# Kernel tuning notes

Measured on AMD Instinct MI355X. Metric: run time of the kernel, lower is better.

The kernel has to match this reference:

```python
import jax, jax.numpy as jnp
import numpy as np

EMBED_DIM = 1024
NUM_HEADS = 16
HEAD_DIM = EMBED_DIM // NUM_HEADS
LAMBDA_ENTANGLE = 0.35


def setup_inputs() -> dict:
    key = jax.random.key(0)
    ks = jax.random.split(key, 10)
    B, S, D = 2, 2048, EMBED_DIM
    init = 1.0 / np.sqrt(D)  # mimic nn.Linear uniform init scale
    x = jax.random.normal(ks[0], (B, S, D), dtype=jnp.float32)
    Wq = jax.random.uniform(ks[1], (D, D), jnp.float32, -init, init)
    bq = jax.random.uniform(ks[2], (D,), jnp.float32, -init, init)
    Wk = jax.random.uniform(ks[3], (D, D), jnp.float32, -init, init)
    bk = jax.random.uniform(ks[4], (D,), jnp.float32, -init, init)
    Wv = jax.random.uniform(ks[5], (D, D), jnp.float32, -init, init)
    bv = jax.random.uniform(ks[6], (D,), jnp.float32, -init, init)
    Wo = jax.random.uniform(ks[7], (D, D), jnp.float32, -init, init)
    bo = jax.random.uniform(ks[8], (D,), jnp.float32, -init, init)
    J_attn = jax.random.normal(ks[9], (NUM_HEADS, HEAD_DIM, HEAD_DIM), dtype=jnp.float32) * 0.02
    lambda_attn = jnp.asarray(LAMBDA_ENTANGLE, dtype=jnp.float32)
    return {"x": x, "Wq": Wq, "bq": bq, "Wk": Wk, "bk": bk, "Wv": Wv, "bv": bv,
            "Wo": Wo, "bo": bo, "J_attn": J_attn, "lambda_attn": lambda_attn}


def reference(x, Wq, bq, Wk, bk, Wv, bv, Wo, bo, J_attn, lambda_attn):
    B, S, D = x.shape
    H, Hd = NUM_HEADS, HEAD_DIM
    scale = jnp.sqrt(jnp.asarray(Hd, dtype=x.dtype))

    def heads(W, b):
        # (B,S,D) @ (D,D) + b -> (B,H,S,Hd)
        y = jnp.einsum('bsd,ed->bse', x, W) + b
        return y.reshape(B, S, H, Hd).transpose(0, 2, 1, 3)

    Q = heads(Wq, bq)
    K = heads(Wk, bk)
    V = heads(Wv, bv)

    scores = jnp.einsum('bhid,bhjd->bhij', Q, K) / scale
    # bilinear entanglement correction: tanh(Q) J tanh(K)^T
    QJ = jnp.einsum('bhid,hde->bhie', jnp.tanh(Q), J_attn)  # (B,H,S,Hd)
    delta = jnp.einsum('bhie,bhje->bhij', QJ, jnp.tanh(K))
    scores = scores + lambda_attn * delta

    causal = jnp.triu(jnp.ones((S, S), dtype=bool), k=1)
    scores = jnp.where(causal, -jnp.inf, scores)

    probs = jax.nn.softmax(scores, axis=-1)
    out = jnp.einsum('bhij,bhjd->bhid', probs, V)  # (B,H,S,Hd)
    out = out.transpose(0, 2, 1, 3).reshape(B, S, D)
    return jnp.einsum('bsd,ed->bse', out, Wo) + bo
```

## Files before the change

### kernel.cpp

```cpp
#include <hip/hip_runtime.h>
#include <hip/hip_bf16.h>

typedef unsigned short u16;
typedef __bf16 bf16x8 __attribute__((ext_vector_type(8)));
typedef float f32x4 __attribute__((ext_vector_type(4)));
typedef unsigned short u16x4 __attribute__((ext_vector_type(4)));

#define MFMA16(a, b, c) __builtin_amdgcn_mfma_f32_16x16x32_bf16(a, b, c, 0, 0, 0)

#define EMB 1024
#define SEQ 2048
#define NH 16
#define HD 64
#define LOG2E 1.4426950408889634f

#define GLOAD_LDS16(g, l) __builtin_amdgcn_global_load_lds( \
    (const __attribute__((address_space(1))) unsigned int*)(g), \
    (__attribute__((address_space(3))) unsigned int*)(l), 16, 0, 0)

__device__ __forceinline__ float b2f(u16 u) {
    union { unsigned int i; float f; } v; v.i = ((unsigned int)u) << 16; return v.f;
}
__device__ __forceinline__ u16 f2b(float f) {
    __hip_bfloat16 h = __float2bfloat16(f);
    return *reinterpret_cast<u16*>(&h);
}
__device__ __forceinline__ u16x4 pack4(float a, float b, float c, float d) {
    union { __hip_bfloat162 h2[2]; u16x4 u; } r;
    r.h2[0] = __float22bfloat162_rn(float2{a, b});
    r.h2[1] = __float22bfloat162_rn(float2{c, d});
    return r.u;
}
__device__ __forceinline__ bf16x8 ldfrag(const u16* p) {
    return *reinterpret_cast<const bf16x8*>(p);
}
__device__ __forceinline__ bf16x8 cvt8(const float* p) {
    const float4 a = *reinterpret_cast<const float4*>(p);
    const float4 b = *reinterpret_cast<const float4*>(p + 4);
    union { u16x4 q[2]; bf16x8 v; } r;
    r.q[0] = pack4(a.x, a.y, a.z, a.w);
    r.q[1] = pack4(b.x, b.y, b.z, b.w);
    return r.v;
}
__device__ __forceinline__ float fast_tanh(float x) {
    float t = __builtin_amdgcn_exp2f(x * (2.0f * LOG2E));
    return 1.0f - 2.0f * __builtin_amdgcn_rcpf(t + 1.0f);
}

__global__ __launch_bounds__(256) void cvt_all(
        const float* __restrict__ x,  const float* __restrict__ Wq,
        const float* __restrict__ Wk, const float* __restrict__ Wv,
        const float* __restrict__ Wo, const float* __restrict__ J,
        u16* __restrict__ dst)
{
    size_t i = ((size_t)blockIdx.x * 256 + threadIdx.x) * 8;
    const float* src; size_t off; u16* d;
    if (i < 4194304) { src = x; off = i; d = dst + i; }
    else if (i < 8388608) {
        size_t j = i - 4194304; int w = (int)(j >> 20); off = j & 1048575;
        src = (w == 0) ? Wq : (w == 1) ? Wk : (w == 2) ? Wv : Wo;
        d = dst + i;
    } else {
        off = i - 8388608; src = J; d = dst + 29360128 + off;
    }
    *(bf16x8*)d = cvt8(src + off);
}

__global__ __launch_bounds__(512) void qkv_fused(
        const u16* __restrict__ A,
        const u16* __restrict__ W0, const float* __restrict__ B0,
        const u16* __restrict__ W1, const float* __restrict__ B1,
        const u16* __restrict__ W2, const float* __restrict__ B2,
        const float* __restrict__ lam, const u16* __restrict__ Jb,
        u16* __restrict__ Qa, u16* __restrict__ Ka, u16* __restrict__ Vt)
{
    __shared__ __attribute__((aligned(16))) u16 sS[2][4][128 * 64];

    const int t = threadIdx.x;
    const int w = t >> 6, L = t & 63;
    const int wm = w >> 1, wn = w & 1;
    const int lr = L & 15, lq = L >> 4;
    const int m0 = blockIdx.y * 128, n0 = blockIdx.x * 128;

    const int c0r = t >> 3,  c0o = ((t & 7) ^ (c0r & 7)) * 8;
    const int c1  = 512 + t;
    const int c1r = c1 >> 3, c1o = ((c1 & 7) ^ (c1r & 7)) * 8;
    const u16* s0p[4], * s1p[4];
    s0p[0] = A  + (size_t)(m0 + c0r) * EMB + c0o;
    s0p[1] = W0 + (size_t)(n0 + c0r) * EMB + c0o;
    s0p[2] = W1 + (size_t)(n0 + c0r) * EMB + c0o;
    s0p[3] = W2 + (size_t)(n0 + c0r) * EMB + c0o;
    s1p[0] = A  + (size_t)(m0 + c1r) * EMB + c1o;
    s1p[1] = W0 + (size_t)(n0 + c1r) * EMB + c1o;
    s1p[2] = W1 + (size_t)(n0 + c1r) * EMB + c1o;
    s1p[3] = W2 + (size_t)(n0 + c1r) * EMB + c1o;

    f32x4 acc[3][2][4];
#pragma unroll
    for (int z = 0; z < 3; z++)
#pragma unroll
        for (int i = 0; i < 2; i++)
#pragma unroll
            for (int j = 0; j < 4; j++) { f32x4 zr = {0.f,0.f,0.f,0.f}; acc[z][i][j] = zr; }

    {
        int4 r0[4], r1[4];
#pragma unroll
        for (int mat = 0; mat < 4; mat++) { r0[mat] = *(const int4*)s0p[mat];
                                            r1[mat] = *(const int4*)s1p[mat]; }
#pragma unroll
        for (int mat = 0; mat < 4; mat++) {
            *(int4*)&sS[0][mat][(size_t)t * 8]  = r0[mat];
            *(int4*)&sS[0][mat][(size_t)c1 * 8] = r1[mat];
        }
    }
    __syncthreads();

    int cur = 0;
    for (int k0 = 0; k0 < EMB; k0 += 64) {
        const bool pf = (k0 + 64) < EMB;
        int4 r0[4], r1[4];
        if (pf) {
#pragma unroll
            for (int mat = 0; mat < 4; mat++) {
                r0[mat] = *(const int4*)(s0p[mat] + k0 + 64);
                r1[mat] = *(const int4*)(s1p[mat] + k0 + 64);
            }
        }
        __builtin_amdgcn_s_setprio(1);
#pragma unroll
        for (int s = 0; s < 2; s++) {
            bf16x8 af[2];
#pragma unroll
            for (int mi = 0; mi < 2; mi++) {
                int row = wm * 32 + mi * 16 + lr;
                af[mi] = ldfrag(&sS[cur][0][(row * 8 + ((s * 4 + lq) ^ (row & 7))) * 8]);
            }
#pragma unroll
            for (int z = 0; z < 3; z++) {
                bf16x8 bfr[4];
#pragma unroll
                for (int ni = 0; ni < 4; ni++) {
                    int row = wn * 64 + ni * 16 + lr;
                    bfr[ni] = ldfrag(
                        &sS[cur][1 + z][(row * 8 + ((s * 4 + lq) ^ (row & 7))) * 8]);
                }
#pragma unroll
                for (int mi = 0; mi < 2; mi++)
#pragma unroll
                    for (int ni = 0; ni < 4; ni++)
                        acc[z][mi][ni] = MFMA16(bfr[ni], af[mi], acc[z][mi][ni]);
            }
        }
        __builtin_amdgcn_s_setprio(0);
        if (pf) {
#pragma unroll
            for (int mat = 0; mat < 4; mat++) {
                *(int4*)&sS[cur ^ 1][mat][(size_t)t * 8]  = r0[mat];
                *(int4*)&sS[cur ^ 1][mat][(size_t)c1 * 8] = r1[mat];
            }
        }
        __syncthreads();
        cur ^= 1;
    }

    u16* sU = &sS[0][0][(size_t)w * 2048];

    const float lamf = lam[0];
    const float qsc = 0.125f * LOG2E, lsc = lamf * LOG2E;
    const float* biases[3] = {B0, B1, B2};
#pragma unroll
    for (int z = 0; z < 3; z++)
#pragma unroll
        for (int mi = 0; mi < 2; mi++)
#pragma unroll
            for (int ni = 0; ni < 4; ni++) {
                const int sg = m0 + wm * 32 + mi * 16 + lr;
                const int ng = n0 + wn * 64 + ni * 16 + lq * 4;
                const float4 bv4 = *(const float4*)&biases[z][ng];
                const float v0 = acc[z][mi][ni][0] + bv4.x;
                const float v1 = acc[z][mi][ni][1] + bv4.y;
                const float v2 = acc[z][mi][ni][2] + bv4.z;
                const float v3 = acc[z][mi][ni][3] + bv4.w;
                const int b = sg >> 11, s0 = sg & 2047;
                const int h = ng >> 6, d0 = ng & 63;
                if (z == 0) {
                    size_t i128 = ((size_t)(b * NH + h) * SEQ + s0) * 128 + d0;
                    *(u16x4*)&Qa[i128] = pack4(v0 * qsc, v1 * qsc, v2 * qsc, v3 * qsc);
                    *(u16x4*)&Qa[i128 + 64] =
                        pack4(lsc * fast_tanh(v0), lsc * fast_tanh(v1),
                              lsc * fast_tanh(v2), lsc * fast_tanh(v3));
                } else if (z == 1) {
                    *(u16x4*)&Ka[((size_t)(b * NH + h) * SEQ + s0) * 128 + d0] =
                        pack4(v0, v1, v2, v3);
                    const int sl = mi * 16 + lr;
                    const int chunk = (d0 >> 3) ^ (sl & 7);
                    *(u16x4*)&sU[sl * 64 + chunk * 8 + (d0 & 7)] =
                        pack4(fast_tanh(v0), fast_tanh(v1),
                              fast_tanh(v2), fast_tanh(v3));
                } else {
#pragma unroll
                    for (int r = 0; r < 4; r++) {
                        float vr = (r == 0) ? v0 : (r == 1) ? v1 : (r == 2) ? v2 : v3;
                        Vt[((size_t)(b * NH + h) * HD + d0 + r) * SEQ + s0] = f2b(vr);
                    }
                }
            }

    {
        const int hn = (n0 >> 6) + wn;
        const u16* Jh = Jb + (size_t)hn * 4096;
        bf16x8 jf[4][2];
#pragma unroll
        for (int nt = 0; nt < 4; nt++)
#pragma unroll
            for (int s2 = 0; s2 < 2; s2++)
                jf[nt][s2] = ldfrag(&Jh[(nt * 16 + lr) * 64 + s2 * 32 + lq * 8]);
#pragma unroll
        for (int rt2 = 0; rt2 < 2; rt2++) {
            const int r32 = rt2 * 16 + lr;
            bf16x8 a0 = ldfrag(&sU[r32 * 64 + ((0 + lq) ^ (r32 & 7)) * 8]);
            bf16x8 a1 = ldfrag(&sU[r32 * 64 + ((4 + lq) ^ (r32 & 7)) * 8]);
            const int grow = m0 + wm * 32 + rt2 * 16 + lr;
            const int bb = grow >> 11, ss = grow & 2047;
            const size_t kbase = ((size_t)(bb * NH + hn) * SEQ + ss) * 128 + 64;
#pragma unroll
            for (int nt = 0; nt < 4; nt++) {
                f32x4 acc2 = {0.f, 0.f, 0.f, 0.f};
                acc2 = MFMA16(jf[nt][0], a0, acc2);
                acc2 = MFMA16(jf[nt][1], a1, acc2);
                *(u16x4*)&Ka[kbase + nt * 16 + lq * 4] =
                    pack4(acc2[0], acc2[1], acc2[2], acc2[3]);
            }
        }
    }
}

template<int MI>
__global__ __launch_bounds__(256, 4) void gemm_epi(
        const u16* __restrict__ A,
        const u16* __restrict__ W0, const float* __restrict__ B0,
        float* __restrict__ out)
{
    const u16* W = W0; const float* bias = B0;

    __shared__ __attribute__((aligned(16))) u16 sA[MI * 32 * 64];
    __shared__ __attribute__((aligned(16))) u16 sB[128 * 64];

    const int t = threadIdx.x;
    const int w = t >> 6, L = t & 63;
    const int wm = w >> 1, wn = w & 1;
    const int lr = L & 15, lq = L >> 4;
    const int wbase = t & 192;
    const int m0 = blockIdx.y * (MI * 32), n0 = blockIdx.x * 128;

    f32x4 acc[MI][4];
#pragma unroll
    for (int i = 0; i < MI; i++)
#pragma unroll
        for (int j = 0; j < 4; j++) { f32x4 z = {0.f, 0.f, 0.f, 0.f}; acc[i][j] = z; }

    for (int k0 = 0; k0 < EMB; k0 += 64) {
        __syncthreads();
#pragma unroll
        for (int q = 0; q < MI; q++) {
            int c = q * 256 + t;
            int row = c >> 3, cc = c & 7;
            int col8 = cc ^ (row & 7);
            GLOAD_LDS16(&A[(size_t)(m0 + row) * EMB + k0 + col8 * 8],
                        &sA[(q * 256 + wbase) * 8]);
        }
#pragma unroll
        for (int q = 0; q < 4; q++) {
            int c = q * 256 + t;
            int row = c >> 3, cc = c & 7;
            int col8 = cc ^ (row & 7);
            GLOAD_LDS16(&W[(size_t)(n0 + row) * EMB + k0 + col8 * 8],
                        &sB[(q * 256 + wbase) * 8]);
        }
        __syncthreads();
#pragma unroll
        for (int s = 0; s < 2; s++) {
            bf16x8 af[MI], bfr[4];
#pragma unroll
            for (int mi = 0; mi < MI; mi++) {
                int row = wm * (MI * 16) + mi * 16 + lr;
                af[mi] = ldfrag(&sA[(row * 8 + ((s * 4 + lq) ^ (row & 7))) * 8]);
            }
#pragma unroll
            for (int ni = 0; ni < 4; ni++) {
                int row = wn * 64 + ni * 16 + lr;
                bfr[ni] = ldfrag(&sB[(row * 8 + ((s * 4 + lq) ^ (row & 7))) * 8]);
            }
#pragma unroll
            for (int mi = 0; mi < MI; mi++)
#pragma unroll
                for (int ni = 0; ni < 4; ni++)
                    acc[mi][ni] = MFMA16(bfr[ni], af[mi], acc[mi][ni]);
        }
    }

#pragma unroll
    for (int mi = 0; mi < MI; mi++)
#pragma unroll
        for (int ni = 0; ni < 4; ni++) {
            const int sg = m0 + wm * (MI * 16) + mi * 16 + lr;
            const int ng = n0 + wn * 64 + ni * 16 + lq * 4;
            const float4 bv4 = *(const float4*)&bias[ng];
            float4 o = {acc[mi][ni][0] + bv4.x, acc[mi][ni][1] + bv4.y,
                        acc[mi][ni][2] + bv4.z, acc[mi][ni][3] + bv4.w};
            *(float4*)&out[(size_t)sg * EMB + ng] = o;
        }
}

__global__ __launch_bounds__(512) void flash(
        const u16* __restrict__ Qa, const u16* __restrict__ Ka,
        const u16* __restrict__ Vt, u16* __restrict__ attn)
{
    __shared__ __attribute__((aligned(16))) u16 sK[2][128 * 128];
    __shared__ __attribute__((aligned(16))) u16 sVt[2][64 * 128];
    __shared__ __attribute__((aligned(16))) u16 sP[128 * 136];
    __shared__ float sLs[2][4][64][2];

    const int t = threadIdx.x, w = t >> 6, L = t & 63, lr = L & 15, lq = L >> 4;
    const int wq = w & 3, wk = w >> 2;
    const int bh = blockIdx.x & 31, p = blockIdx.x >> 5;
    const int i_l = wq * 16 + lr;
    const u16* Kbase = Ka + (size_t)bh * SEQ * 128;
    const u16* Vbase = Vt + (size_t)bh * HD * SEQ;
    const int b = bh >> 4, h = bh & 15;
    float* sOt = reinterpret_cast<float*>(sK);

    const u16* kq[4];
#pragma unroll
    for (int q = 0; q < 4; q++) {
        int c = q * 512 + t;
        int row = c >> 4, cc = c & 15;
        kq[q] = Kbase + (size_t)row * 128 + (cc ^ (row & 15)) * 8;
    }
    const u16* vq[2];
#pragma unroll
    for (int q = 0; q < 2; q++) {
        int c = q * 512 + t;
        int d = c >> 4, cc = c & 15;
        vq[q] = Vbase + (size_t)d * SEQ + (cc ^ (d & 7)) * 8;
    }

#pragma unroll 1
    for (int seg = 0; seg < 2; seg++) {
        const int qt = seg ? 15 - p : p;
        const int qm = qt * 128;

        bf16x8 qf[2][4];
#pragma unroll
        for (int g = 0; g < 2; g++) {
            const u16* qrow = Qa + ((size_t)bh * SEQ + qm + g * 64 + i_l) * 128;
#pragma unroll
            for (int s = 0; s < 4; s++) qf[g][s] = ldfrag(qrow + s * 32 + lq * 8);
        }

        f32x4 Ot[2][4];
#pragma unroll
        for (int g = 0; g < 2; g++)
#pragma unroll
            for (int i = 0; i < 4; i++) { f32x4 z = {0.f, 0.f, 0.f, 0.f}; Ot[g][i] = z; }
        float lsum[2] = {0.f, 0.f};

        {
            int4 a0 = *(const int4*)kq[0];
            int4 a1 = *(const int4*)kq[1];
            int4 a2 = *(const int4*)kq[2];
            int4 a3 = *(const int4*)kq[3];
            int4 b0 = *(const int4*)vq[0];
            int4 b1 = *(const int4*)vq[1];
            *(int4*)&sK[0][(size_t)(0 * 512 + t) * 8] = a0;
            *(int4*)&sK[0][(size_t)(1 * 512 + t) * 8] = a1;
            *(int4*)&sK[0][(size_t)(2 * 512 + t) * 8] = a2;
            *(int4*)&sK[0][(size_t)(3 * 512 + t) * 8] = a3;
            *(int4*)&sVt[0][(size_t)(0 * 512 + t) * 8] = b0;
            *(int4*)&sVt[0][(size_t)(1 * 512 + t) * 8] = b1;
        }
        __syncthreads();

        int cur = 0;
        for (int kt = 0; kt <= qt; kt++) {
            const bool pf = kt < qt;
            int4 rk0, rk1, rk2, rk3, rv0, rv1;
            if (pf) {
                const int kn = (kt + 1) * 128;
                rk0 = *(const int4*)(kq[0] + (size_t)kn * 128);
                rk1 = *(const int4*)(kq[1] + (size_t)kn * 128);
                rk2 = *(const int4*)(kq[2] + (size_t)kn * 128);
                rk3 = *(const int4*)(kq[3] + (size_t)kn * 128);
                rv0 = *(const int4*)(vq[0] + kn);
                rv1 = *(const int4*)(vq[1] + kn);
            }
            const u16* sKc = sK[cur];
            const u16* sVc = sVt[cur];

            f32x4 sc[2][4];
#pragma unroll
            for (int g = 0; g < 2; g++)
#pragma unroll
                for (int m = 0; m < 4; m++) { f32x4 z = {0.f,0.f,0.f,0.f}; sc[g][m] = z; }
            __builtin_amdgcn_s_setprio(1);
#pragma unroll
            for (int mt2 = 0; mt2 < 4; mt2++) {
                int j = wk * 64 + mt2 * 16 + lr;
#pragma unroll
                for (int s = 0; s < 4; s++) {
                    bf16x8 kf = ldfrag(&sKc[(j * 16 + ((s * 4 + lq) ^ (j & 15))) * 8]);
                    sc[0][mt2] = MFMA16(kf, qf[0][s], sc[0][mt2]);
                    sc[1][mt2] = MFMA16(kf, qf[1][s], sc[1][mt2]);
                }
            }
            __builtin_amdgcn_s_setprio(0);
            if (kt == qt) {
#pragma unroll
                for (int mt2 = 0; mt2 < 4; mt2++)
#pragma unroll
                    for (int r = 0; r < 4; r++) {
                        int jj = wk * 64 + mt2 * 16 + lq * 4 + r;
                        if (jj > i_l)      sc[0][mt2][r] = -INFINITY;
                        if (jj > 64 + i_l) sc[1][mt2][r] = -INFINITY;
                    }
            }
#pragma unroll
            for (int g = 0; g < 2; g++) {
#pragma unroll
                for (int mt2 = 0; mt2 < 4; mt2++) {
                    float e0 = __builtin_amdgcn_exp2f(sc[g][mt2][0]);
                    float e1 = __builtin_amdgcn_exp2f(sc[g][mt2][1]);
                    float e2 = __builtin_amdgcn_exp2f(sc[g][mt2][2]);
                    float e3 = __builtin_amdgcn_exp2f(sc[g][mt2][3]);
                    lsum[g] += (e0 + e1) + (e2 + e3);
                    *(u16x4*)&sP[(g * 64 + i_l) * 136 + wk * 64 + mt2 * 16 + lq * 4] =
                        pack4(e0, e1, e2, e3);
                }
            }
            __builtin_amdgcn_s_setprio(1);
#pragma unroll
            for (int s2l = 0; s2l < 2; s2l++) {
                bf16x8 pf0 = ldfrag(&sP[(i_l) * 136 + wk * 64 + s2l * 32 + lq * 8]);
                bf16x8 pf1 = ldfrag(&sP[(64 + i_l) * 136 + wk * 64 + s2l * 32 + lq * 8]);
#pragma unroll
                for (int mt = 0; mt < 4; mt++) {
                    int d = mt * 16 + lr;
                    bf16x8 vf = ldfrag(
                        &sVc[(d * 16 + ((wk * 8 + s2l * 4 + lq) ^ (d & 7))) * 8]);
                    Ot[0][mt] = MFMA16(vf, pf0, Ot[0][mt]);
                    Ot[1][mt] = MFMA16(vf, pf1, Ot[1][mt]);
                }
            }
            __builtin_amdgcn_s_setprio(0);
            if (pf) {
                *(int4*)&sK[cur ^ 1][(size_t)(0 * 512 + t) * 8] = rk0;
                *(int4*)&sK[cur ^ 1][(size_t)(1 * 512 + t) * 8] = rk1;
                *(int4*)&sK[cur ^ 1][(size_t)(2 * 512 + t) * 8] = rk2;
                *(int4*)&sK[cur ^ 1][(size_t)(3 * 512 + t) * 8] = rk3;
                *(int4*)&sVt[cur ^ 1][(size_t)(0 * 512 + t) * 8] = rv0;
                *(int4*)&sVt[cur ^ 1][(size_t)(1 * 512 + t) * 8] = rv1;
            }
            __syncthreads();
            cur ^= 1;
        }

#pragma unroll
        for (int g = 0; g < 2; g++) {
            lsum[g] += __shfl_xor(lsum[g], 16);
            lsum[g] += __shfl_xor(lsum[g], 32);
            sLs[wk][wq][L][g] = lsum[g];
        }
        if (wk == 1) {
            float* dst = &sOt[wq * 64 + L];
#pragma unroll
            for (int g = 0; g < 2; g++)
#pragma unroll
                for (int mt = 0; mt < 4; mt++)
#pragma unroll
                    for (int r = 0; r < 4; r++)
                        dst[256 * (g * 16 + mt * 4 + r)] = Ot[g][mt][r];
        }
        __syncthreads();
        if (wk == 0) {
            const float* src = &sOt[wq * 64 + L];
#pragma unroll
            for (int g = 0; g < 2; g++) {
                float ls = lsum[g] + sLs[1][wq][L][g];
                const float r0 = __builtin_amdgcn_rcpf(ls);
                const float inv = r0 * (2.0f - ls * r0);
                const size_t base =
                    ((size_t)(b * SEQ + qm + g * 64 + i_l)) * EMB + h * HD;
#pragma unroll
                for (int mt = 0; mt < 4; mt++)
                    *(u16x4*)&attn[base + mt * 16 + lq * 4] = pack4(
                        (Ot[g][mt][0] + src[256 * (g * 16 + mt * 4 + 0)]) * inv,
                        (Ot[g][mt][1] + src[256 * (g * 16 + mt * 4 + 1)]) * inv,
                        (Ot[g][mt][2] + src[256 * (g * 16 + mt * 4 + 2)]) * inv,
                        (Ot[g][mt][3] + src[256 * (g * 16 + mt * 4 + 3)]) * inv);
            }
        }
        __syncthreads();
    }
}

extern "C" void kernel_launch(void* const* d_in, const int* in_sizes, int n_in,
                              void* d_out, int out_size, void* d_ws, size_t ws_size,
                              hipStream_t stream)
{
    const float* x   = (const float*)d_in[0];
    const float* Wq  = (const float*)d_in[1];
    const float* bq  = (const float*)d_in[2];
    const float* Wk  = (const float*)d_in[3];
    const float* bk  = (const float*)d_in[4];
    const float* Wv  = (const float*)d_in[5];
    const float* bv  = (const float*)d_in[6];
    const float* Wo  = (const float*)d_in[7];
    const float* bo  = (const float*)d_in[8];
    const float* J   = (const float*)d_in[9];
    const float* lam = (const float*)d_in[10];

    u16* ws  = (u16*)d_ws;
    u16* xb  = ws;
    u16* Wqb = xb  + (size_t)4096 * 1024;
    u16* Wkb = Wqb + (size_t)1024 * 1024;
    u16* Wvb = Wkb + (size_t)1024 * 1024;
    u16* Wob = Wvb + (size_t)1024 * 1024;
    u16* Qa  = Wob + (size_t)1024 * 1024;
    u16* Ka  = Qa  + (size_t)32 * 2048 * 128;
    u16* Vt  = Ka  + (size_t)32 * 2048 * 128;
    u16* Jb  = Vt  + (size_t)32 * 64 * 2048;
    u16* attn = xb;
    float* dout = (float*)d_out;

    dim3 blk(256);
    cvt_all<<<dim3(4128), blk, 0, stream>>>(x, Wq, Wk, Wv, Wo, J, ws);
    qkv_fused<<<dim3(8, 32), dim3(512), 0, stream>>>(
        xb, Wqb, bq, Wkb, bk, Wvb, bv, lam, Jb, Qa, Ka, Vt);
    flash<<<dim3(256), dim3(512), 0, stream>>>(Qa, Ka, Vt, attn);
    gemm_epi<2><<<dim3(8, 64), blk, 0, stream>>>(attn, Wob, bo, dout);
}
```

Baseline: 221.4 us.

## Split fused QKV GEMM into per-projection blocks with smaller tiles

Replaces the fused QKV kernel, where each 512-thread block computed all three projections for a 128x128 tile, with a 256-thread kernel that takes the projection index from blockIdx.z and covers a 64x128 tile. The grid grows from 256 to 1536 blocks and per-thread accumulator and LDS use shrink, so occupancy and load balance across CUs should improve. The cost is that the activation tile is no longer shared across Q, K and V, so it is reloaded three times. The software pipeline also changes: sched_barriers replace setprio, and the last iteration issues a redundant load instead of a branch.

```diff
diff --git a/kernel.cpp b/kernel.cpp
--- a/kernel.cpp
+++ b/kernel.cpp
@@ -66,7 +66,7 @@
     *(bf16x8*)d = cvt8(src + off);
 }
 
-__global__ __launch_bounds__(512) void qkv_fused(
+__global__ __launch_bounds__(256, 3) void qkv_gemm(
         const u16* __restrict__ A,
         const u16* __restrict__ W0, const float* __restrict__ B0,
         const u16* __restrict__ W1, const float* __restrict__ B1,
@@ -74,140 +74,142 @@
         const float* __restrict__ lam, const u16* __restrict__ Jb,
         u16* __restrict__ Qa, u16* __restrict__ Ka, u16* __restrict__ Vt)
 {
-    __shared__ __attribute__((aligned(16))) u16 sS[2][4][128 * 64];
+    const int mode = blockIdx.z;
+    const u16* W; const float* bias;
+    if (mode == 0)      { W = W0; bias = B0; }
+    else if (mode == 1) { W = W1; bias = B1; }
+    else                { W = W2; bias = B2; }
+
+    __shared__ __attribute__((aligned(16))) u16 sA[2][64 * 64];
+    __shared__ __attribute__((aligned(16))) u16 sB[2][128 * 64];
 
     const int t = threadIdx.x;
     const int w = t >> 6, L = t & 63;
     const int wm = w >> 1, wn = w & 1;
     const int lr = L & 15, lq = L >> 4;
-    const int m0 = blockIdx.y * 128, n0 = blockIdx.x * 128;
-
-    const int c0r = t >> 3,  c0o = ((t & 7) ^ (c0r & 7)) * 8;
-    const int c1  = 512 + t;
-    const int c1r = c1 >> 3, c1o = ((c1 & 7) ^ (c1r & 7)) * 8;
-    const u16* s0p[4], * s1p[4];
-    s0p[0] = A  + (size_t)(m0 + c0r) * EMB + c0o;
-    s0p[1] = W0 + (size_t)(n0 + c0r) * EMB + c0o;
-    s0p[2] = W1 + (size_t)(n0 + c0r) * EMB + c0o;
-    s0p[3] = W2 + (size_t)(n0 + c0r) * EMB + c0o;
-    s1p[0] = A  + (size_t)(m0 + c1r) * EMB + c1o;
-    s1p[1] = W0 + (size_t)(n0 + c1r) * EMB + c1o;
-    s1p[2] = W1 + (size_t)(n0 + c1r) * EMB + c1o;
-    s1p[3] = W2 + (size_t)(n0 + c1r) * EMB + c1o;
-
-    f32x4 acc[3][2][4];
-#pragma unroll
-    for (int z = 0; z < 3; z++)
-#pragma unroll
-        for (int i = 0; i < 2; i++)
-#pragma unroll
-            for (int j = 0; j < 4; j++) { f32x4 zr = {0.f,0.f,0.f,0.f}; acc[z][i][j] = zr; }
+    const int m0 = blockIdx.y * 64, n0 = blockIdx.x * 128;
+
+    const u16* aptr[2];
+#pragma unroll
+    for (int q = 0; q < 2; q++) {
+        int c = q * 256 + t;
+        int row = c >> 3, col8 = (c & 7) ^ (row & 7);
+        aptr[q] = &A[(size_t)(m0 + row) * EMB + col8 * 8];
+    }
+    const u16* bptr[4];
+#pragma unroll
+    for (int q = 0; q < 4; q++) {
+        int c = q * 256 + t;
+        int row = c >> 3, col8 = (c & 7) ^ (row & 7);
+        bptr[q] = &W[(size_t)(n0 + row) * EMB + col8 * 8];
+    }
+
+    f32x4 acc[2][4];
+#pragma unroll
+    for (int i = 0; i < 2; i++)
+#pragma unroll
+        for (int j = 0; j < 4; j++) { f32x4 z = {0.f, 0.f, 0.f, 0.f}; acc[i][j] = z; }
 
     {
-        int4 r0[4], r1[4];
-#pragma unroll
-        for (int mat = 0; mat < 4; mat++) { r0[mat] = *(const int4*)s0p[mat];
-                                            r1[mat] = *(const int4*)s1p[mat]; }
-#pragma unroll
-        for (int mat = 0; mat < 4; mat++) {
-            *(int4*)&sS[0][mat][(size_t)t * 8]  = r0[mat];
-            *(int4*)&sS[0][mat][(size_t)c1 * 8] = r1[mat];
-        }
+        int4 ra0 = *(const int4*)aptr[0];
+        int4 ra1 = *(const int4*)aptr[1];
+        int4 rb0 = *(const int4*)bptr[0];
+        int4 rb1 = *(const int4*)bptr[1];
+        int4 rb2 = *(const int4*)bptr[2];
+        int4 rb3 = *(const int4*)bptr[3];
+        *(int4*)&sA[0][(size_t)(0 * 256 + t) * 8] = ra0;
+        *(int4*)&sA[0][(size_t)(1 * 256 + t) * 8] = ra1;
+        *(int4*)&sB[0][(size_t)(0 * 256 + t) * 8] = rb0;
+        *(int4*)&sB[0][(size_t)(1 * 256 + t) * 8] = rb1;
+        *(int4*)&sB[0][(size_t)(2 * 256 + t) * 8] = rb2;
+        *(int4*)&sB[0][(size_t)(3 * 256 + t) * 8] = rb3;
     }
     __syncthreads();
 
     int cur = 0;
     for (int k0 = 0; k0 < EMB; k0 += 64) {
-        const bool pf = (k0 + 64) < EMB;
-        int4 r0[4], r1[4];
-        if (pf) {
-#pragma unroll
-            for (int mat = 0; mat < 4; mat++) {
-                r0[mat] = *(const int4*)(s0p[mat] + k0 + 64);
-                r1[mat] = *(const int4*)(s1p[mat] + k0 + 64);
-            }
-        }
-        __builtin_amdgcn_s_setprio(1);
+        const int kn = (k0 + 64 < EMB) ? (k0 + 64) : k0;
+        int4 ra0 = *(const int4*)(aptr[0] + kn);
+        int4 ra1 = *(const int4*)(aptr[1] + kn);
+        int4 rb0 = *(const int4*)(bptr[0] + kn);
+        int4 rb1 = *(const int4*)(bptr[1] + kn);
+        int4 rb2 = *(const int4*)(bptr[2] + kn);
+        int4 rb3 = *(const int4*)(bptr[3] + kn);
+        __builtin_amdgcn_sched_barrier(0);
+
+        const u16* sAc = sA[cur];
+        const u16* sBc = sB[cur];
 #pragma unroll
         for (int s = 0; s < 2; s++) {
-            bf16x8 af[2];
+            bf16x8 af[2], bfr[4];
 #pragma unroll
             for (int mi = 0; mi < 2; mi++) {
                 int row = wm * 32 + mi * 16 + lr;
-                af[mi] = ldfrag(&sS[cur][0][(row * 8 + ((s * 4 + lq) ^ (row & 7))) * 8]);
-            }
-#pragma unroll
-            for (int z = 0; z < 3; z++) {
-                bf16x8 bfr[4];
-#pragma unroll
-                for (int ni = 0; ni < 4; ni++) {
-                    int row = wn * 64 + ni * 16 + lr;
-                    bfr[ni] = ldfrag(
-                        &sS[cur][1 + z][(row * 8 + ((s * 4 + lq) ^ (row & 7))) * 8]);
-                }
-#pragma unroll
-                for (int mi = 0; mi < 2; mi++)
-#pragma unroll
-                    for (int ni = 0; ni < 4; ni++)
-                        acc[z][mi][ni] = MFMA16(bfr[ni], af[mi], acc[z][mi][ni]);
-            }
-        }
-        __builtin_amdgcn_s_setprio(0);
-        if (pf) {
-#pragma unroll
-            for (int mat = 0; mat < 4; mat++) {
-                *(int4*)&sS[cur ^ 1][mat][(size_t)t * 8]  = r0[mat];
-                *(int4*)&sS[cur ^ 1][mat][(size_t)c1 * 8] = r1[mat];
-            }
-        }
+                af[mi] = ldfrag(&sAc[(row * 8 + ((s * 4 + lq) ^ (row & 7))) * 8]);
+            }
+#pragma unroll
+            for (int ni = 0; ni < 4; ni++) {
+                int row = wn * 64 + ni * 16 + lr;
+                bfr[ni] = ldfrag(&sBc[(row * 8 + ((s * 4 + lq) ^ (row & 7))) * 8]);
+            }
+#pragma unroll
+            for (int mi = 0; mi < 2; mi++)
+#pragma unroll
+                for (int ni = 0; ni < 4; ni++)
+                    acc[mi][ni] = MFMA16(bfr[ni], af[mi], acc[mi][ni]);
+        }
+        __builtin_amdgcn_sched_barrier(0);
+        *(int4*)&sA[cur ^ 1][(size_t)(0 * 256 + t) * 8] = ra0;
+        *(int4*)&sA[cur ^ 1][(size_t)(1 * 256 + t) * 8] = ra1;
+        *(int4*)&sB[cur ^ 1][(size_t)(0 * 256 + t) * 8] = rb0;
+        *(int4*)&sB[cur ^ 1][(size_t)(1 * 256 + t) * 8] = rb1;
+        *(int4*)&sB[cur ^ 1][(size_t)(2 * 256 + t) * 8] = rb2;
+        *(int4*)&sB[cur ^ 1][(size_t)(3 * 256 + t) * 8] = rb3;
         __syncthreads();
         cur ^= 1;
     }
 
-    u16* sU = &sS[0][0][(size_t)w * 2048];
+    u16* sU = &sB[0][(size_t)w * 2048];
 
     const float lamf = lam[0];
     const float qsc = 0.125f * LOG2E, lsc = lamf * LOG2E;
-    const float* biases[3] = {B0, B1, B2};
-#pragma unroll
-    for (int z = 0; z < 3; z++)
-#pragma unroll
-        for (int mi = 0; mi < 2; mi++)
-#pragma unroll
-            for (int ni = 0; ni < 4; ni++) {
-                const int sg = m0 + wm * 32 + mi * 16 + lr;
-                const int ng = n0 + wn * 64 + ni * 16 + lq * 4;
-                const float4 bv4 = *(const float4*)&biases[z][ng];
-                const float v0 = acc[z][mi][ni][0] + bv4.x;
-                const float v1 = acc[z][mi][ni][1] + bv4.y;
-                const float v2 = acc[z][mi][ni][2] + bv4.z;
-                const float v3 = acc[z][mi][ni][3] + bv4.w;
-                const int b = sg >> 11, s0 = sg & 2047;
-                const int h = ng >> 6, d0 = ng & 63;
-                if (z == 0) {
-                    size_t i128 = ((size_t)(b * NH + h) * SEQ + s0) * 128 + d0;
-                    *(u16x4*)&Qa[i128] = pack4(v0 * qsc, v1 * qsc, v2 * qsc, v3 * qsc);
-                    *(u16x4*)&Qa[i128 + 64] =
-                        pack4(lsc * fast_tanh(v0), lsc * fast_tanh(v1),
-                              lsc * fast_tanh(v2), lsc * fast_tanh(v3));
-                } else if (z == 1) {
-                    *(u16x4*)&Ka[((size_t)(b * NH + h) * SEQ + s0) * 128 + d0] =
-                        pack4(v0, v1, v2, v3);
-                    const int sl = mi * 16 + lr;
-                    const int chunk = (d0 >> 3) ^ (sl & 7);
-                    *(u16x4*)&sU[sl * 64 + chunk * 8 + (d0 & 7)] =
-                        pack4(fast_tanh(v0), fast_tanh(v1),
-                              fast_tanh(v2), fast_tanh(v3));
-                } else {
-#pragma unroll
-                    for (int r = 0; r < 4; r++) {
-                        float vr = (r == 0) ? v0 : (r == 1) ? v1 : (r == 2) ? v2 : v3;
-                        Vt[((size_t)(b * NH + h) * HD + d0 + r) * SEQ + s0] = f2b(vr);
-                    }
+#pragma unroll
+    for (int mi = 0; mi < 2; mi++)
+#pragma unroll
+        for (int ni = 0; ni < 4; ni++) {
+            const int sg = m0 + wm * 32 + mi * 16 + lr;
+            const int ng = n0 + wn * 64 + ni * 16 + lq * 4;
+            const float4 bv4 = *(const float4*)&bias[ng];
+            const float v0 = acc[mi][ni][0] + bv4.x;
+            const float v1 = acc[mi][ni][1] + bv4.y;
+            const float v2 = acc[mi][ni][2] + bv4.z;
+            const float v3 = acc[mi][ni][3] + bv4.w;
+            const int b = sg >> 11, s0 = sg & 2047;
+            const int h = ng >> 6, d0 = ng & 63;
+            if (mode == 0) {
+                size_t i128 = ((size_t)(b * NH + h) * SEQ + s0) * 128 + d0;
+                *(u16x4*)&Qa[i128] = pack4(v0 * qsc, v1 * qsc, v2 * qsc, v3 * qsc);
+                *(u16x4*)&Qa[i128 + 64] =
+                    pack4(lsc * fast_tanh(v0), lsc * fast_tanh(v1),
+                          lsc * fast_tanh(v2), lsc * fast_tanh(v3));
+            } else if (mode == 1) {
+                *(u16x4*)&Ka[((size_t)(b * NH + h) * SEQ + s0) * 128 + d0] =
+                    pack4(v0, v1, v2, v3);
+                const int sl = mi * 16 + lr;
+                const int chunk = (d0 >> 3) ^ (sl & 7);
+                *(u16x4*)&sU[sl * 64 + chunk * 8 + (d0 & 7)] =
+                    pack4(fast_tanh(v0), fast_tanh(v1),
+                          fast_tanh(v2), fast_tanh(v3));
+            } else {
+#pragma unroll
+                for (int r = 0; r < 4; r++) {
+                    float vr = (r == 0) ? v0 : (r == 1) ? v1 : (r == 2) ? v2 : v3;
+                    Vt[((size_t)(b * NH + h) * HD + d0 + r) * SEQ + s0] = f2b(vr);
                 }
             }
-
-    {
+        }
+
+    if (mode == 1) {
         const int hn = (n0 >> 6) + wn;
         const u16* Jh = Jb + (size_t)hn * 4096;
         bf16x8 jf[4][2];
@@ -535,7 +537,7 @@
 
     dim3 blk(256);
     cvt_all<<<dim3(4128), blk, 0, stream>>>(x, Wq, Wk, Wv, Wo, J, ws);
-    qkv_fused<<<dim3(8, 32), dim3(512), 0, stream>>>(
+    qkv_gemm<<<dim3(8, 64, 3), blk, 0, stream>>>(
         xb, Wqb, bq, Wkb, bk, Wvb, bv, lam, Jb, Qa, Ka, Vt);
     flash<<<dim3(256), dim3(512), 0, stream>>>(Qa, Ka, Vt, attn);
     gemm_epi<2><<<dim3(8, 64), blk, 0, stream>>>(attn, Wob, bo, dout);
```

Measured after the change: 195.8 us. 1.13x faster.
